# Performance work log

Measured on AMD Instinct MI355X. Metric: run time of the kernel, lower is better.

Reference implementation:

```python
import jax, jax.numpy as jnp
import numpy as np

SIZE = 48
DIST = 6
PAD = DIST // 2
DESIZE = SIZE - 4  # 44
CONVEY = 0.9
RATE = 5
BATCH = 4
FLAT = DESIZE * SIZE * SIZE  # 101376


def setup_inputs() -> dict:
    key = jax.random.key(0)
    ks = jax.random.split(key, 6)
    D, H, W = DESIZE, SIZE, SIZE
    return {
        "vinput": jax.random.normal(ks[0], (BATCH, D, H, W), jnp.float32),
        "frame": jax.random.normal(ks[1], (D, H, W), jnp.float32) * 0.1,
        # 0.05 scale keeps the 216-term recurrent sums ~unit magnitude over RATE steps
        "synapse": jax.random.normal(ks[2], (D, H, W, DIST, DIST, DIST), jnp.float32) * 0.05,
        "W1": jax.random.normal(ks[3], (FLAT, 1024), jnp.float32) * 0.01,
        "b1": jnp.zeros((1024,), jnp.float32),
        "W2": jax.random.normal(ks[4], (1024, 128), jnp.float32) * 0.05,
        "b2": jnp.zeros((128,), jnp.float32),
        "W3": jax.random.normal(ks[5], (128, 10), jnp.float32) * 0.1,
        "b3": jnp.zeros((10,), jnp.float32),
    }


def _local_step(neu, syn_flat, d, p):
    """Locally-connected (unshared-weight) 3D window reduce.
    neu: (B, D, H, W); syn_flat: (D, H, W, d^3).
    For each voxel, weighted sum over its d x d x d padded neighborhood."""
    B, D, H, W = neu.shape
    pad = jnp.pad(neu, ((0, 0), (p, p), (p, p), (p, p)))
    # patches: (B, d^3, D', H', W') with valid windows; keep the first D/H/W starts
    patches = jax.lax.conv_general_dilated_patches(
        pad[:, None], filter_shape=(d, d, d), window_strides=(1, 1, 1), padding="VALID"
    )
    patches = patches[:, :, :D, :H, :W]
    return jnp.einsum("bcijk,ijkc->bijk", patches, syn_flat)


def reference(vinput, frame, synapse, W1, b1, W2, b2, W3, b3):
    D, H, W = frame.shape
    d = synapse.shape[-1]
    p = d // 2
    syn_flat = synapse.reshape(D, H, W, d * d * d)
    neu = vinput + frame  # frame broadcast over batch
    for _ in range(RATE):
        out = _local_step(neu, syn_flat, d, p)
        neu = jax.nn.relu(out) * CONVEY
    x = neu.reshape(neu.shape[0], -1)
    x = jax.nn.relu(x @ W1 + b1)
    x = jax.nn.relu(x @ W2 + b2)
    return x @ W3 + b3
```

## Files before the change

kernel.cpp:

```cpp
#include <hip/hip_runtime.h>

#define SIZE   48
#define DESIZE 44
#define PAD    3
#define BATCH  4
#define FLAT   (DESIZE*SIZE*SIZE)
#define CVOL   216

#define TJ 4
#define TK 16
#define NA 6
#define NB (TJ+5)
#define NC (TK+5)
#define NEU_T (NA*NB*NC)
#define SYN_PITCH 217

#define KSLICE  96
#define NSLICES (FLAT/KSLICE)

template <int W>
__device__ __forceinline__ void do_chunk4(const float* __restrict__ sl,
                                          const float* __restrict__ neu_t,
                                          int lanebase, float acc[4]) {
#pragma unroll
    for (int s = 0; s < 54; ++s) {
        const int c  = W * 54 + s;
        const int fd = c / 36;
        const int fh = (c % 36) / 6;
        const int fw = c % 6;
        const int off = lanebase + fd * (NB * NC) + fh * NC + fw;
        float w = sl[c];
        const float4 n4 = *(const float4*)(neu_t + off * 4);
        acc[0] += w * n4.x;
        acc[1] += w * n4.y;
        acc[2] += w * n4.z;
        acc[3] += w * n4.w;
    }
}

template <bool FIRST>
__global__ __launch_bounds__(256) void k_step(const float* __restrict__ nin,
                                              const float* __restrict__ vin,
                                              const float* __restrict__ frame,
                                              const float* __restrict__ syn,
                                              float* __restrict__ nout) {
    __shared__ float syn_t[64 * SYN_PITCH];
    __shared__ float neu_t[NEU_T * 4];
    __shared__ float part[4 * 256];
    int t = threadIdx.x;
    int r  = blockIdx.x;
    int i0 = r / 36;
    int r2 = r % 36;
    int j0 = (r2 / 3) * TJ;
    int k0 = (r2 % 3) * TK;

    for (int e = t; e < 64 * (CVOL / 4); e += 256) {
        int v = e / 54, c4 = e % 54;
        int dj = v >> 4, dk = v & 15;
        const float4* s4 = (const float4*)(syn +
            (size_t)((i0 * SIZE + j0 + dj) * SIZE + k0 + dk) * CVOL);
        float4 val = s4[c4];
        float* dst = syn_t + v * SYN_PITCH + c4 * 4;
        dst[0] = val.x; dst[1] = val.y; dst[2] = val.z; dst[3] = val.w;
    }
    for (int e = t; e < NEU_T; e += 256) {
        int a   = e / (NB * NC);
        int rem = e % (NB * NC);
        int jj  = rem / NC;
        int cc  = rem % NC;
        int gi = i0 + a - PAD;
        int gj = j0 + jj - PAD;
        int gk = k0 + cc - PAD;
        float4 vv = make_float4(0.f, 0.f, 0.f, 0.f);
        if ((unsigned)gi < DESIZE && (unsigned)gj < SIZE && (unsigned)gk < SIZE) {
            int idx = (gi * SIZE + gj) * SIZE + gk;
            if (FIRST) {
                float fr = frame[idx];
                vv.x = vin[0 * FLAT + idx] + fr;
                vv.y = vin[1 * FLAT + idx] + fr;
                vv.z = vin[2 * FLAT + idx] + fr;
                vv.w = vin[3 * FLAT + idx] + fr;
            } else {
                vv.x = nin[0 * FLAT + idx];
                vv.y = nin[1 * FLAT + idx];
                vv.z = nin[2 * FLAT + idx];
                vv.w = nin[3 * FLAT + idx];
            }
        }
        *(float4*)(neu_t + e * 4) = vv;
    }
    __syncthreads();

    int w = t >> 6, l = t & 63;
    int dj = l >> 4, dk = l & 15;
    int lanebase = dj * NC + dk;
    const float* sl = syn_t + l * SYN_PITCH;
    float acc[4] = {0.f, 0.f, 0.f, 0.f};
    switch (w) {
        case 0:  do_chunk4<0>(sl, neu_t, lanebase, acc); break;
        case 1:  do_chunk4<1>(sl, neu_t, lanebase, acc); break;
        case 2:  do_chunk4<2>(sl, neu_t, lanebase, acc); break;
        default: do_chunk4<3>(sl, neu_t, lanebase, acc); break;
    }
#pragma unroll
    for (int bb = 0; bb < 4; ++bb) part[bb * 256 + t] = acc[bb];
    __syncthreads();

    {
        int bb = t >> 6, lv = t & 63;
        float s = part[bb * 256 + lv] + part[bb * 256 + 64 + lv] +
                  part[bb * 256 + 128 + lv] + part[bb * 256 + 192 + lv];
        s = fmaxf(s, 0.f) * 0.9f;
        int dj2 = lv >> 4, dk2 = lv & 15;
        nout[(size_t)bb * FLAT + (i0 * SIZE + (j0 + dj2)) * SIZE + (k0 + dk2)] = s;
    }
}

__global__ __launch_bounds__(256) void k_mlp1(const float* __restrict__ xc,
                                              const float* __restrict__ W1,
                                              float* __restrict__ partial) {
    __shared__ float xs[KSLICE * 4];
    int t = threadIdx.x;
    int s = blockIdx.x;
    int k0 = s * KSLICE;
    for (int e = t; e < KSLICE * 4; e += 256) {
        int kk = e >> 2, b = e & 3;
        xs[e] = xc[(size_t)b * FLAT + k0 + kk];
    }
    __syncthreads();
    float acc[4][4] = {};
    const float* wp = W1 + (size_t)k0 * 1024 + t * 4;
#pragma unroll 8
    for (int kk = 0; kk < KSLICE; ++kk) {
        float4 w  = *(const float4*)(wp + (size_t)kk * 1024);
        float4 xv = *(const float4*)(xs + kk * 4);
        acc[0][0] += xv.x * w.x; acc[0][1] += xv.x * w.y; acc[0][2] += xv.x * w.z; acc[0][3] += xv.x * w.w;
        acc[1][0] += xv.y * w.x; acc[1][1] += xv.y * w.y; acc[1][2] += xv.y * w.z; acc[1][3] += xv.y * w.w;
        acc[2][0] += xv.z * w.x; acc[2][1] += xv.z * w.y; acc[2][2] += xv.z * w.z; acc[2][3] += xv.z * w.w;
        acc[3][0] += xv.w * w.x; acc[3][1] += xv.w * w.y; acc[3][2] += xv.w * w.z; acc[3][3] += xv.w * w.w;
    }
#pragma unroll
    for (int b = 0; b < 4; ++b) {
        float4 o = make_float4(acc[b][0], acc[b][1], acc[b][2], acc[b][3]);
        *(float4*)(partial + (size_t)s * 4096 + b * 1024 + t * 4) = o;
    }
}

__global__ __launch_bounds__(256) void k_reduce1(const float* __restrict__ partial,
                                                 const float* __restrict__ b1,
                                                 float* __restrict__ h1) {
    __shared__ float red[16][17];
    int t = threadIdx.x;
    int e0 = blockIdx.x * 16;
    int eo = t & 15, sl = t >> 4;
    float acc = 0.f;
    for (int it = 0; it < NSLICES / 16; ++it) {
        int s = sl + 16 * it;
        acc += partial[(size_t)s * 4096 + e0 + eo];
    }
    red[sl][eo] = acc;
    __syncthreads();
    if (t < 16) {
        float a = 0.f;
#pragma unroll
        for (int rr = 0; rr < 16; ++rr) a += red[rr][t];
        int e = e0 + t;
        h1[e] = fmaxf(a + b1[e & 1023], 0.f);
    }
}

__global__ __launch_bounds__(64) void k_mlp2(const float* __restrict__ h1,
                                             const float* __restrict__ W2,
                                             float* __restrict__ partial2) {
    __shared__ float xs[128 * 4];
    int t = threadIdx.x;
    int bid = blockIdx.x;
    int s = bid >> 1, ch = bid & 1;
    int k0 = s * 128;
    for (int e = t; e < 512; e += 64) {
        int kk = e >> 2, b = e & 3;
        xs[e] = h1[b * 1024 + k0 + kk];
    }
    __syncthreads();
    float acc[4] = {0.f, 0.f, 0.f, 0.f};
    int n2 = ch * 64 + t;
    for (int kk = 0; kk < 128; ++kk) {
        float w = W2[(k0 + kk) * 128 + n2];
        float4 xv = *(const float4*)(xs + kk * 4);
        acc[0] += xv.x * w; acc[1] += xv.y * w; acc[2] += xv.z * w; acc[3] += xv.w * w;
    }
#pragma unroll
    for (int b = 0; b < 4; ++b) partial2[s * 512 + b * 128 + n2] = acc[b];
}

__global__ __launch_bounds__(128) void k_mlp3(const float* __restrict__ partial2,
                                              const float* __restrict__ b2,
                                              const float* __restrict__ W3,
                                              const float* __restrict__ b3,
                                              float* __restrict__ out) {
    __shared__ float h2[512];
    int t = threadIdx.x;
    for (int e = t; e < 512; e += 128) {
        int n2 = e & 127;
        float a = b2[n2];
        for (int s = 0; s < 8; ++s) a += partial2[s * 512 + e];
        h2[e] = fmaxf(a, 0.f);
    }
    __syncthreads();
    if (t < 40) {
        int b = t / 10, o = t % 10;
        float a = b3[o];
        for (int k = 0; k < 128; ++k) a += h2[b * 128 + k] * W3[k * 10 + o];
        out[b * 10 + o] = a;
    }
}

extern "C" void kernel_launch(void* const* d_in, const int* in_sizes, int n_in,
                              void* d_out, int out_size, void* d_ws, size_t ws_size,
                              hipStream_t stream) {
    const float* vin   = (const float*)d_in[0];
    const float* frame = (const float*)d_in[1];
    const float* syn   = (const float*)d_in[2];
    const float* W1    = (const float*)d_in[3];
    const float* b1    = (const float*)d_in[4];
    const float* W2    = (const float*)d_in[5];
    const float* b2    = (const float*)d_in[6];
    const float* W3    = (const float*)d_in[7];
    const float* b3    = (const float*)d_in[8];
    float* out = (float*)d_out;

    float* ws = (float*)d_ws;
    float* A   = ws;
    float* B   = A + (size_t)BATCH * FLAT;
    float* P1  = B + (size_t)BATCH * FLAT;
    float* H1  = P1 + (size_t)NSLICES * 4096;
    float* P2  = H1 + 4096;

    k_step<true ><<<1584, 256, 0, stream>>>(nullptr, vin, frame, syn, A);
    k_step<false><<<1584, 256, 0, stream>>>(A, nullptr, nullptr, syn, B);
    k_step<false><<<1584, 256, 0, stream>>>(B, nullptr, nullptr, syn, A);
    k_step<false><<<1584, 256, 0, stream>>>(A, nullptr, nullptr, syn, B);
    k_step<false><<<1584, 256, 0, stream>>>(B, nullptr, nullptr, syn, A);

    k_mlp1<<<NSLICES, 256, 0, stream>>>(A, W1, P1);
    k_reduce1<<<256, 256, 0, stream>>>(P1, b1, H1);
    k_mlp2<<<16, 64, 0, stream>>>(H1, W2, P2);
    k_mlp3<<<1, 128, 0, stream>>>(P2, b2, W3, b3, out);
}
```

Before: 784.8 us.

## Load synapse weights directly into registers and widen MLP2 split

The step kernel no longer stages the 64x216 synapse tile through shared memory. Each thread now reads its own float4 chunk of synapse weights straight from global memory into registers, which removes about 55 KB of LDS, a sync-bound staging loop and the bank-conflict-padded pitch, and adds an occupancy hint of 4 blocks per CU. Each thread's global reads are strided by 864 bytes across lanes, so coalescing is poor, though every byte is used once. Separately, MLP2 is split into 64 blocks over 32-element K slices instead of 16 blocks, and MLP3 now reduces 32 partials instead of 8.

```diff
diff --git a/kernel.cpp b/kernel.cpp
--- a/kernel.cpp
+++ b/kernel.cpp
@@ -13,56 +13,51 @@
 #define NB (TJ+5)
 #define NC (TK+5)
 #define NEU_T (NA*NB*NC)
-#define SYN_PITCH 217
 
 #define KSLICE  96
 #define NSLICES (FLAT/KSLICE)
 
-template <int W>
-__device__ __forceinline__ void do_chunk4(const float* __restrict__ sl,
-                                          const float* __restrict__ neu_t,
+template <int CBASE, int CNT>
+__device__ __forceinline__ void do_chunk4(const float4* __restrict__ rp,
+                                          const float4* __restrict__ neu4,
                                           int lanebase, float acc[4]) {
-#pragma unroll
-    for (int s = 0; s < 54; ++s) {
-        const int c  = W * 54 + s;
-        const int fd = c / 36;
-        const int fh = (c % 36) / 6;
-        const int fw = c % 6;
-        const int off = lanebase + fd * (NB * NC) + fh * NC + fw;
-        float w = sl[c];
-        const float4 n4 = *(const float4*)(neu_t + off * 4);
-        acc[0] += w * n4.x;
-        acc[1] += w * n4.y;
-        acc[2] += w * n4.z;
-        acc[3] += w * n4.w;
+    float4 sr[CNT];
+#pragma unroll
+    for (int s = 0; s < CNT; ++s) sr[s] = rp[CBASE + s];
+#pragma unroll
+    for (int s = 0; s < CNT; ++s) {
+#pragma unroll
+        for (int j = 0; j < 4; ++j) {
+            const int c  = (CBASE + s) * 4 + j;
+            const int fd = c / 36;
+            const int fh = (c % 36) / 6;
+            const int fw = c % 6;
+            const int off = fd * (NB * NC) + fh * NC + fw;
+            const float wv = (&sr[s].x)[j];
+            const float4 n4 = neu4[lanebase + off];
+            acc[0] += wv * n4.x;
+            acc[1] += wv * n4.y;
+            acc[2] += wv * n4.z;
+            acc[3] += wv * n4.w;
+        }
     }
 }
 
 template <bool FIRST>
-__global__ __launch_bounds__(256) void k_step(const float* __restrict__ nin,
-                                              const float* __restrict__ vin,
-                                              const float* __restrict__ frame,
-                                              const float* __restrict__ syn,
-                                              float* __restrict__ nout) {
-    __shared__ float syn_t[64 * SYN_PITCH];
-    __shared__ float neu_t[NEU_T * 4];
-    __shared__ float part[4 * 256];
-    int t = threadIdx.x;
+__global__ __launch_bounds__(256, 4) void k_step(const float* __restrict__ nin,
+                                                 const float* __restrict__ vin,
+                                                 const float* __restrict__ frame,
+                                                 const float* __restrict__ syn,
+                                                 float* __restrict__ nout) {
+    __shared__ float4 neu4[NEU_T];
+    __shared__ float  part[4 * 256];
+    int t  = threadIdx.x;
     int r  = blockIdx.x;
     int i0 = r / 36;
     int r2 = r % 36;
     int j0 = (r2 / 3) * TJ;
     int k0 = (r2 % 3) * TK;
 
-    for (int e = t; e < 64 * (CVOL / 4); e += 256) {
-        int v = e / 54, c4 = e % 54;
-        int dj = v >> 4, dk = v & 15;
-        const float4* s4 = (const float4*)(syn +
-            (size_t)((i0 * SIZE + j0 + dj) * SIZE + k0 + dk) * CVOL);
-        float4 val = s4[c4];
-        float* dst = syn_t + v * SYN_PITCH + c4 * 4;
-        dst[0] = val.x; dst[1] = val.y; dst[2] = val.z; dst[3] = val.w;
-    }
     for (int e = t; e < NEU_T; e += 256) {
         int a   = e / (NB * NC);
         int rem = e % (NB * NC);
@@ -87,20 +82,22 @@
                 vv.w = nin[3 * FLAT + idx];
             }
         }
-        *(float4*)(neu_t + e * 4) = vv;
+        neu4[e] = vv;
     }
     __syncthreads();
 
     int w = t >> 6, l = t & 63;
     int dj = l >> 4, dk = l & 15;
     int lanebase = dj * NC + dk;
-    const float* sl = syn_t + l * SYN_PITCH;
+    const float4* rp = (const float4*)(syn +
+        (size_t)((i0 * SIZE + j0 + dj) * SIZE + k0 + dk) * CVOL);
+
     float acc[4] = {0.f, 0.f, 0.f, 0.f};
     switch (w) {
-        case 0:  do_chunk4<0>(sl, neu_t, lanebase, acc); break;
-        case 1:  do_chunk4<1>(sl, neu_t, lanebase, acc); break;
-        case 2:  do_chunk4<2>(sl, neu_t, lanebase, acc); break;
-        default: do_chunk4<3>(sl, neu_t, lanebase, acc); break;
+        case 0:  do_chunk4< 0, 14>(rp, neu4, lanebase, acc); break;
+        case 1:  do_chunk4<14, 14>(rp, neu4, lanebase, acc); break;
+        case 2:  do_chunk4<28, 13>(rp, neu4, lanebase, acc); break;
+        default: do_chunk4<41, 13>(rp, neu4, lanebase, acc); break;
     }
 #pragma unroll
     for (int bb = 0; bb < 4; ++bb) part[bb * 256 + t] = acc[bb];
@@ -172,20 +169,21 @@
 __global__ __launch_bounds__(64) void k_mlp2(const float* __restrict__ h1,
                                              const float* __restrict__ W2,
                                              float* __restrict__ partial2) {
-    __shared__ float xs[128 * 4];
+    __shared__ float xs[32 * 4];
     int t = threadIdx.x;
     int bid = blockIdx.x;
     int s = bid >> 1, ch = bid & 1;
-    int k0 = s * 128;
-    for (int e = t; e < 512; e += 64) {
+    int k0 = s * 32;
+    for (int e = t; e < 128; e += 64) {
         int kk = e >> 2, b = e & 3;
         xs[e] = h1[b * 1024 + k0 + kk];
     }
     __syncthreads();
     float acc[4] = {0.f, 0.f, 0.f, 0.f};
     int n2 = ch * 64 + t;
-    for (int kk = 0; kk < 128; ++kk) {
-        float w = W2[(k0 + kk) * 128 + n2];
+#pragma unroll
+    for (int kk = 0; kk < 32; ++kk) {
+        float w = W2[(size_t)(k0 + kk) * 128 + n2];
         float4 xv = *(const float4*)(xs + kk * 4);
         acc[0] += xv.x * w; acc[1] += xv.y * w; acc[2] += xv.z * w; acc[3] += xv.w * w;
     }
@@ -203,7 +201,8 @@
     for (int e = t; e < 512; e += 128) {
         int n2 = e & 127;
         float a = b2[n2];
-        for (int s = 0; s < 8; ++s) a += partial2[s * 512 + e];
+#pragma unroll 8
+        for (int s = 0; s < 32; ++s) a += partial2[s * 512 + e];
         h2[e] = fmaxf(a, 0.f);
     }
     __syncthreads();
@@ -244,6 +243,6 @@
 
     k_mlp1<<<NSLICES, 256, 0, stream>>>(A, W1, P1);
     k_reduce1<<<256, 256, 0, stream>>>(P1, b1, H1);
-    k_mlp2<<<16, 64, 0, stream>>>(H1, W2, P2);
+    k_mlp2<<<64, 64, 0, stream>>>(H1, W2, P2);
     k_mlp3<<<1, 128, 0, stream>>>(P2, b2, W3, b3, out);
 }
```

Measured after the change: 719.7 us. 8.3% less time.
